# Kernel optimization log

Measured on AMD Instinct MI355X. Metric: run time of the kernel, lower is better.

The kernel has to match this reference:

```python
import jax, jax.numpy as jnp
import numpy as np

_FRAC_BITS = 8  # assumed fixed-point fractional bits for bits_quant
_SCALE = float(2 ** _FRAC_BITS)

def bits_quant(x):
    # Simulated fixed-point quantization: round to nearest multiple of 2^-8.
    return jnp.round(x * _SCALE) / _SCALE


def setup_inputs() -> dict:
    key = jax.random.key(0)
    k1, k2, k3 = jax.random.split(key, 3)
    B, D_in, D_out = 4096, 4096, 4096
    inputs = jax.random.normal(k1, (B, D_in), dtype=jnp.float32)
    w = jax.random.normal(k2, (D_in, D_out), dtype=jnp.float32) * 0.02
    b = jax.random.normal(k3, (D_out,), dtype=jnp.float32) * 0.02
    return {"inputs": inputs, "w": w, "b": b}


def reference(inputs, w, b):
    # y = bits_quant(inputs @ w) + bits_quant(b); out = bits_quant(y)
    y = bits_quant(jnp.matmul(inputs, w)) + bits_quant(b)
    return bits_quant(y)
```

## Files before the change

kernel.cpp:

```cpp
#include <hip/hip_runtime.h>
#include <math.h>

typedef __attribute__((ext_vector_type(8))) short   short8;
typedef __attribute__((ext_vector_type(4))) float   f32x4;
typedef __attribute__((ext_vector_type(4))) float   float4v;
typedef __attribute__((ext_vector_type(8))) unsigned short ushort8;
typedef __attribute__((ext_vector_type(4))) unsigned short ushort4v;

#define NDIM 4096
#define BK   64

__device__ __forceinline__ unsigned short f2bf(float f) {
  unsigned u = __builtin_bit_cast(unsigned, f);
  u += 0x7fffu + ((u >> 16) & 1u);
  return (unsigned short)(u >> 16);
}

__device__ __forceinline__ void gload_lds16(const unsigned short* g, unsigned short* l) {
  __builtin_amdgcn_global_load_lds(
      (const __attribute__((address_space(1))) void*)g,
      (__attribute__((address_space(3))) void*)l, 16, 0, 0);
}

__global__ void prep(const float* __restrict__ A, unsigned short* __restrict__ Abf,
                     const float* __restrict__ W, unsigned short* __restrict__ Wt) {
  __shared__ unsigned short tileb[64][68];
  const int t = threadIdx.x;
  if (blockIdx.x < 8192) {
    int i = (blockIdx.x * 256 + t) * 8;
    float4v a = *(const float4v*)(A + i);
    float4v b = *(const float4v*)(A + i + 4);
    ushort8 o;
    o[0] = f2bf(a[0]); o[1] = f2bf(a[1]); o[2] = f2bf(a[2]); o[3] = f2bf(a[3]);
    o[4] = f2bf(b[0]); o[5] = f2bf(b[1]); o[6] = f2bf(b[2]); o[7] = f2bf(b[3]);
    *(ushort8*)(Abf + i) = o;
  } else {
    int b  = blockIdx.x - 8192;
    int n0 = (b & 63) * 64, k0 = (b >> 6) * 64;
    const int rr = t >> 4;
    const int cc = (t & 15) * 4;
#pragma unroll
    for (int i = 0; i < 4; ++i) {
      int k = rr + i * 16;
      float4v v = *(const float4v*)&W[(size_t)(k0 + k) * NDIM + n0 + cc];
      ushort4v u;
      u[0] = f2bf(v[0]); u[1] = f2bf(v[1]); u[2] = f2bf(v[2]); u[3] = f2bf(v[3]);
      *(ushort4v*)&tileb[k][cc] = u;
    }
    __syncthreads();
#pragma unroll
    for (int i = 0; i < 2; ++i) {
      int c  = t + i * 256;
      int n  = c >> 3;
      int kc = (c & 7) * 8;
      ushort8 v;
#pragma unroll
      for (int j = 0; j < 8; ++j) v[j] = tileb[kc + j][n];
      *(ushort8*)&Wt[(size_t)(n0 + n) * NDIM + k0 + kc] = v;
    }
  }
}

__global__ __launch_bounds__(256, 4)
void gemm_bt_quant(const unsigned short* __restrict__ A,
                   const unsigned short* __restrict__ Bt,
                   const float* __restrict__ bias,
                   float* __restrict__ C) {
  __shared__ unsigned short As[128 * BK];
  __shared__ unsigned short Bs[128 * BK];

  const int tid  = threadIdx.x;
  const int lane = tid & 63;
  const int wid  = tid >> 6;
  const int wm   = (wid >> 1) * 64;
  const int wn   = (wid & 1) * 64;
  const int m0   = blockIdx.y * 128;
  const int n0   = blockIdx.x * 128;

  const int srow = tid >> 3;
  const int sc   = (tid & 7) ^ ((srow & 1) * 4);
  const unsigned short* Ag = A  + (size_t)(m0 + srow) * NDIM + sc * 8;
  const unsigned short* Bg = Bt + (size_t)(n0 + srow) * NDIM + sc * 8;

  const int frow = lane & 15;
  const int fk   = (lane >> 4) * 8;
  const int fpar = frow & 1;

  f32x4 acc[4][4] = {};

  for (int kt = 0; kt < NDIM; kt += BK) {
#pragma unroll
    for (int p = 0; p < 4; ++p) {
      gload_lds16(Ag + kt + (size_t)p * 32 * NDIM, &As[(p * 256 + tid) * 8]);
      gload_lds16(Bg + kt + (size_t)p * 32 * NDIM, &Bs[(p * 256 + tid) * 8]);
    }
    __syncthreads();

#pragma unroll
    for (int h = 0; h < 2; ++h) {
      const int ko = fk + 32 * (h ^ fpar);
      short8 af[4], bfr[4];
#pragma unroll
      for (int i = 0; i < 4; ++i)
        af[i] = *(const short8*)&As[(wm + i * 16 + frow) * BK + ko];
#pragma unroll
      for (int j = 0; j < 4; ++j)
        bfr[j] = *(const short8*)&Bs[(wn + j * 16 + frow) * BK + ko];
#pragma unroll
      for (int i = 0; i < 4; ++i)
#pragma unroll
        for (int j = 0; j < 4; ++j)
          acc[i][j] = __builtin_amdgcn_mfma_f32_16x16x32_bf16(af[i], bfr[j], acc[i][j], 0, 0, 0);
    }

    __syncthreads();
  }

  const float inv = 1.0f / 256.0f;
  const int colb = n0 + wn + (lane & 15);
  const int rowb = m0 + wm + (lane >> 4) * 4;
#pragma unroll
  for (int j = 0; j < 4; ++j) {
    const int col = colb + j * 16;
    const float qb = rintf(bias[col] * 256.0f) * inv;
#pragma unroll
    for (int i = 0; i < 4; ++i) {
      float* Cp = C + (size_t)(rowb + i * 16) * NDIM + col;
#pragma unroll
      for (int r = 0; r < 4; ++r)
        Cp[(size_t)r * NDIM] = rintf(acc[i][j][r] * 256.0f) * inv + qb;
    }
  }
}

__global__ void gemm_fb(const float* __restrict__ A, const float* __restrict__ W,
                        const float* __restrict__ bias, float* __restrict__ C) {
  __shared__ float As[32][33], Ws[32][33];
  int tx = threadIdx.x, ty = threadIdx.y;
  int m0 = blockIdx.y * 32, n0 = blockIdx.x * 32;
  float acc[4] = {0.f, 0.f, 0.f, 0.f};
  for (int k0 = 0; k0 < NDIM; k0 += 32) {
#pragma unroll
    for (int i = 0; i < 4; ++i) {
      int r = ty + i * 8;
      As[r][tx] = A[(size_t)(m0 + r) * NDIM + k0 + tx];
      Ws[r][tx] = W[(size_t)(k0 + r) * NDIM + n0 + tx];
    }
    __syncthreads();
#pragma unroll
    for (int k = 0; k < 32; ++k) {
      float wv = Ws[k][tx];
#pragma unroll
      for (int i = 0; i < 4; ++i) acc[i] += As[ty + i * 8][k] * wv;
    }
    __syncthreads();
  }
  float qb = rintf(bias[n0 + tx] * 256.0f) * (1.0f / 256.0f);
#pragma unroll
  for (int i = 0; i < 4; ++i)
    C[(size_t)(m0 + ty + i * 8) * NDIM + n0 + tx] =
        rintf(acc[i] * 256.0f) * (1.0f / 256.0f) + qb;
}

extern "C" void kernel_launch(void* const* d_in, const int* in_sizes, int n_in,
                              void* d_out, int out_size, void* d_ws, size_t ws_size,
                              hipStream_t stream) {
  const float* A    = (const float*)d_in[0];
  const float* W    = (const float*)d_in[1];
  const float* bias = (const float*)d_in[2];
  float* C = (float*)d_out;
  const size_t nElem = (size_t)NDIM * NDIM;

  if (ws_size >= nElem * 4) {
    unsigned short* Abf = (unsigned short*)d_ws;
    unsigned short* Wt  = Abf + nElem;
    prep<<<8192 + 4096, 256, 0, stream>>>(A, Abf, W, Wt);
    gemm_bt_quant<<<dim3(32, 32), 256, 0, stream>>>(Abf, Wt, bias, C);
  } else {
    gemm_fb<<<dim3(128, 128), dim3(32, 8), 0, stream>>>(A, W, bias, C);
  }
}
```

Measured before the change: 311.8 us.

## Enlarge GEMM tile to 256x128 and switch to 32x32x16 MFMA with XOR swizzle

Grows each block's output tile from 128x128 to 256x128, so each wave computes 128x64 using 32x32x16 bf16 MFMAs in place of 16x16x32. This raises arithmetic intensity per LDS fragment load and cuts global/LDS traffic per FLOP. The LDS layout moves to a full 8-way XOR swizzle to avoid bank conflicts for the new fragment access pattern. In exchange, occupancy drops (launch bounds 2), the grid has only 512 blocks, and the epilogue stores are more scattered per lane.

```diff
diff --git a/kernel.cpp b/kernel.cpp
--- a/kernel.cpp
+++ b/kernel.cpp
@@ -1,14 +1,16 @@
 #include <hip/hip_runtime.h>
 #include <math.h>
 
-typedef __attribute__((ext_vector_type(8))) short   short8;
-typedef __attribute__((ext_vector_type(4))) float   f32x4;
-typedef __attribute__((ext_vector_type(4))) float   float4v;
-typedef __attribute__((ext_vector_type(8))) unsigned short ushort8;
-typedef __attribute__((ext_vector_type(4))) unsigned short ushort4v;
+typedef __attribute__((ext_vector_type(8)))  short  short8;
+typedef __attribute__((ext_vector_type(16))) float  f32x16;
+typedef __attribute__((ext_vector_type(4)))  float  float4v;
+typedef __attribute__((ext_vector_type(8)))  unsigned short ushort8;
+typedef __attribute__((ext_vector_type(4)))  unsigned short ushort4v;
 
 #define NDIM 4096
-#define BK   64
+#define BM 256
+#define BN 128
+#define BK 64
 
 __device__ __forceinline__ unsigned short f2bf(float f) {
   unsigned u = __builtin_bit_cast(unsigned, f);
@@ -61,74 +63,74 @@
   }
 }
 
-__global__ __launch_bounds__(256, 4)
+__global__ __launch_bounds__(256, 2)
 void gemm_bt_quant(const unsigned short* __restrict__ A,
                    const unsigned short* __restrict__ Bt,
                    const float* __restrict__ bias,
                    float* __restrict__ C) {
-  __shared__ unsigned short As[128 * BK];
-  __shared__ unsigned short Bs[128 * BK];
+  __shared__ unsigned short As[BM * BK];
+  __shared__ unsigned short Bs[BN * BK];
 
   const int tid  = threadIdx.x;
   const int lane = tid & 63;
   const int wid  = tid >> 6;
-  const int wm   = (wid >> 1) * 64;
+  const int wm   = (wid >> 1) * 128;
   const int wn   = (wid & 1) * 64;
-  const int m0   = blockIdx.y * 128;
-  const int n0   = blockIdx.x * 128;
+  const int m0   = blockIdx.y * BM;
+  const int n0   = blockIdx.x * BN;
 
   const int srow = tid >> 3;
-  const int sc   = (tid & 7) ^ ((srow & 1) * 4);
+  const int sc   = (tid & 7) ^ (srow & 7);
   const unsigned short* Ag = A  + (size_t)(m0 + srow) * NDIM + sc * 8;
   const unsigned short* Bg = Bt + (size_t)(n0 + srow) * NDIM + sc * 8;
 
-  const int frow = lane & 15;
-  const int fk   = (lane >> 4) * 8;
-  const int fpar = frow & 1;
+  const int fr = lane & 31;
+  const int fh = lane >> 5;
+  const int fsw = fr & 7;
 
-  f32x4 acc[4][4] = {};
+  f32x16 acc[4][2] = {};
 
   for (int kt = 0; kt < NDIM; kt += BK) {
 #pragma unroll
-    for (int p = 0; p < 4; ++p) {
-      gload_lds16(Ag + kt + (size_t)p * 32 * NDIM, &As[(p * 256 + tid) * 8]);
-      gload_lds16(Bg + kt + (size_t)p * 32 * NDIM, &Bs[(p * 256 + tid) * 8]);
-    }
+    for (int p = 0; p < 8; ++p)
+      gload_lds16(Ag + kt + (size_t)(p * 32) * NDIM, &As[(p * 256 + tid) * 8]);
+#pragma unroll
+    for (int p = 0; p < 4; ++p)
+      gload_lds16(Bg + kt + (size_t)(p * 32) * NDIM, &Bs[(p * 256 + tid) * 8]);
     __syncthreads();
 
 #pragma unroll
-    for (int h = 0; h < 2; ++h) {
-      const int ko = fk + 32 * (h ^ fpar);
-      short8 af[4], bfr[4];
+    for (int h = 0; h < 4; ++h) {
+      const int cph = (2 * h + fh) ^ fsw;
+      short8 af[4], bfr[2];
 #pragma unroll
       for (int i = 0; i < 4; ++i)
-        af[i] = *(const short8*)&As[(wm + i * 16 + frow) * BK + ko];
+        af[i] = *(const short8*)&As[(wm + i * 32 + fr) * BK + cph * 8];
 #pragma unroll
-      for (int j = 0; j < 4; ++j)
-        bfr[j] = *(const short8*)&Bs[(wn + j * 16 + frow) * BK + ko];
+      for (int j = 0; j < 2; ++j)
+        bfr[j] = *(const short8*)&Bs[(wn + j * 32 + fr) * BK + cph * 8];
 #pragma unroll
       for (int i = 0; i < 4; ++i)
 #pragma unroll
-        for (int j = 0; j < 4; ++j)
-          acc[i][j] = __builtin_amdgcn_mfma_f32_16x16x32_bf16(af[i], bfr[j], acc[i][j], 0, 0, 0);
+        for (int j = 0; j < 2; ++j)
+          acc[i][j] = __builtin_amdgcn_mfma_f32_32x32x16_bf16(af[i], bfr[j], acc[i][j], 0, 0, 0);
     }
-
     __syncthreads();
   }
 
   const float inv = 1.0f / 256.0f;
-  const int colb = n0 + wn + (lane & 15);
-  const int rowb = m0 + wm + (lane >> 4) * 4;
 #pragma unroll
-  for (int j = 0; j < 4; ++j) {
-    const int col = colb + j * 16;
+  for (int j = 0; j < 2; ++j) {
+    const int col = n0 + wn + j * 32 + fr;
     const float qb = rintf(bias[col] * 256.0f) * inv;
 #pragma unroll
     for (int i = 0; i < 4; ++i) {
-      float* Cp = C + (size_t)(rowb + i * 16) * NDIM + col;
+      const int rb = m0 + wm + i * 32 + 4 * fh;
 #pragma unroll
-      for (int r = 0; r < 4; ++r)
-        Cp[(size_t)r * NDIM] = rintf(acc[i][j][r] * 256.0f) * inv + qb;
+      for (int r = 0; r < 16; ++r) {
+        const int row = rb + (r & 3) + 8 * (r >> 2);
+        C[(size_t)row * NDIM + col] = rintf(acc[i][j][r] * 256.0f) * inv + qb;
+      }
     }
   }
 }
@@ -175,7 +177,7 @@
     unsigned short* Abf = (unsigned short*)d_ws;
     unsigned short* Wt  = Abf + nElem;
     prep<<<8192 + 4096, 256, 0, stream>>>(A, Abf, W, Wt);
-    gemm_bt_quant<<<dim3(32, 32), 256, 0, stream>>>(Abf, Wt, bias, C);
+    gemm_bt_quant<<<dim3(NDIM / BN, NDIM / BM), 256, 0, stream>>>(Abf, Wt, bias, C);
   } else {
     gemm_fb<<<dim3(128, 128), dim3(32, 8), 0, stream>>>(A, W, bias, C);
   }
```

Measured after the change: 299.5 us. 1.04x faster.
